# Kernel optimization log

Measured on AMD Instinct MI355X. Metric: run time of the kernel, lower is better.

## Reference

```python
import jax, jax.numpy as jnp
import numpy as np

D_MODEL = 1024
NUM_HEADS = 16
D_K = D_MODEL // NUM_HEADS
ROPE_THETA = 10000.0


def apply_rope(x, pos):
    # x: [B, H, S, d_k], pos: [S] int
    half = x.shape[-1] // 2
    inv_freq = ROPE_THETA ** (-jnp.arange(half, dtype=jnp.float32) * 2.0 / x.shape[-1])
    ang = pos.astype(jnp.float32)[:, None] * inv_freq[None, :]  # [S, half]
    cos, sin = jnp.cos(ang), jnp.sin(ang)
    x1 = x[..., 0::2]
    x2 = x[..., 1::2]
    r1 = x1 * cos - x2 * sin
    r2 = x1 * sin + x2 * cos
    return jnp.stack([r1, r2], axis=-1).reshape(x.shape)


def setup_inputs() -> dict:
    key = jax.random.key(0)
    ks = jax.random.split(key, 5)
    B, S = 4, 2048
    scale = 1.0 / np.sqrt(D_MODEL)
    x = jax.random.normal(ks[0], (B, S, D_MODEL), dtype=jnp.float32)
    w_q = jax.random.normal(ks[1], (D_MODEL, D_MODEL), dtype=jnp.float32) * scale
    w_k = jax.random.normal(ks[2], (D_MODEL, D_MODEL), dtype=jnp.float32) * scale
    w_v = jax.random.normal(ks[3], (D_MODEL, D_MODEL), dtype=jnp.float32) * scale
    w_o = jax.random.normal(ks[4], (D_MODEL, D_MODEL), dtype=jnp.float32) * scale
    token_positions = jnp.arange(S, dtype=jnp.int32)
    return {"x": x, "w_q": w_q, "w_k": w_k, "w_v": w_v, "w_o": w_o, "token_positions": token_positions}


def reference(x, w_q, w_k, w_v, w_o, token_positions):
    B, S, _ = x.shape
    def proj(w):
        return (x @ w.T).reshape(B, S, NUM_HEADS, D_K).transpose(0, 2, 1, 3)  # [B,H,S,d_k]
    q, k, v = proj(w_q), proj(w_k), proj(w_v)
    q = apply_rope(q, token_positions)
    k = apply_rope(k, token_positions)
    logits = jnp.einsum('bhid,bhjd->bhij', q, k) / jnp.sqrt(jnp.float32(D_K))
    causal = jnp.tril(jnp.ones((S, S), dtype=bool))
    logits = jnp.where(causal[None, None], logits, -jnp.inf)
    weights = jax.nn.softmax(logits, axis=-1)
    attn = jnp.einsum('bhij,bhjd->bhid', weights, v)  # [B,H,S,d_k]
    attn = attn.transpose(0, 2, 1, 3).reshape(B, S, D_MODEL)
    return attn @ w_o.T
```

## Files before the change

kernel.cpp:

```cpp
#include <hip/hip_runtime.h>
#include <hip/hip_bf16.h>
#include <stdint.h>

#define DM   1024
#define SEQ  2048
#define BATCH 4
#define NH   16
#define DK   64
#define NTK  16

typedef __attribute__((ext_vector_type(8))) __bf16 bf16x8;
typedef __attribute__((ext_vector_type(4))) float f32x4;
typedef __attribute__((ext_vector_type(4))) unsigned short ushort4_t;
typedef __attribute__((ext_vector_type(4))) unsigned int uint4_t;

typedef __attribute__((address_space(1))) const unsigned int GU32;
typedef __attribute__((address_space(3))) unsigned int LU32;

__device__ inline void gl_lds16(const void* g, void* l) {
  __builtin_amdgcn_global_load_lds((GU32*)g, (LU32*)l, 16, 0, 0);
}

__device__ inline f32x4 mfma16(bf16x8 a, bf16x8 b, f32x4 c) {
  return __builtin_amdgcn_mfma_f32_16x16x32_bf16(a, b, c, 0, 0, 0);
}

__device__ inline unsigned short f2bf(float f) {
  unsigned u = __float_as_uint(f);
  u += 0x7fffu + ((u >> 16) & 1u);
  return (unsigned short)(u >> 16);
}

__device__ inline unsigned cvt_pk_bf16(float a, float b) {
  unsigned r;
  asm("v_cvt_pk_bf16_f32 %0, %1, %2" : "=v"(r) : "v"(a), "v"(b));
  return r;
}

__device__ inline float fexp2(float x) {
  float r;
  asm("v_exp_f32 %0, %1" : "=v"(r) : "v"(x));
  return r;
}

__device__ inline float fmax3(float a, float b, float c) {
  float r;
  asm("v_max3_f32 %0, %1, %2, %3" : "=v"(r) : "v"(a), "v"(b), "v"(c));
  return r;
}

__device__ inline int swz_of(int r) { return ((r & 6) << 2) | ((r & 1) << 5); }
__device__ inline int bswz(int r) { return ((r & 6) << 3) | ((r & 1) << 6); }

__global__ void prep_kernel(const float* __restrict__ x,
                            const float* __restrict__ wq, const float* __restrict__ wk,
                            const float* __restrict__ wv, const float* __restrict__ wo,
                            const int* __restrict__ tp,
                            unsigned short* __restrict__ xbf,
                            unsigned short* __restrict__ wbf,
                            float2* __restrict__ tab)
{
  const int NX4 = (BATCH*SEQ*DM)/4;
  const int NW4 = (DM*DM)/4;
  int idx = blockIdx.x*256 + threadIdx.x;
  if (idx < NX4) {
    float4 v = ((const float4*)x)[idx];
    ushort4_t o; o[0]=f2bf(v.x); o[1]=f2bf(v.y); o[2]=f2bf(v.z); o[3]=f2bf(v.w);
    ((ushort4_t*)xbf)[idx] = o;
  } else if (idx < NX4 + 4*NW4) {
    int t = idx - NX4;
    int wsel = t >> 18;
    int off = t & (NW4-1);
    const float* src = (wsel==0) ? wq : (wsel==1) ? wk : (wsel==2) ? wv : wo;
    float4 v = ((const float4*)src)[off];
    ushort4_t o; o[0]=f2bf(v.x); o[1]=f2bf(v.y); o[2]=f2bf(v.z); o[3]=f2bf(v.w);
    ((ushort4_t*)wbf)[wsel*NW4 + off] = o;
  } else {
    int t = idx - NX4 - 4*NW4;
    if (t < SEQ*32) {
      int s = t >> 5, i = t & 31;
      float invf = exp2f(-(float)i * (13.287712379549449f/32.0f));
      float ang = (float)tp[s] * invf;
      float sn, cs; sincosf(ang, &sn, &cs);
      tab[t] = make_float2(cs, sn);
    }
  }
}

template<int MODE>
__global__ __launch_bounds__(256, 2)
void gemm_db(const unsigned short* __restrict__ A,
             const unsigned short* __restrict__ Wall,
             unsigned short* __restrict__ qbf,
             unsigned short* __restrict__ kbf,
             unsigned short* __restrict__ vt,
             float* __restrict__ ofp,
             const float2* __restrict__ tab)
{
  __shared__ __align__(16) char lds[65536];
  const int tid = threadIdx.x;
  const int bid = blockIdx.x;
  int sel, mt, nt;
  if (MODE == 0) {
    sel = bid >> 9;
    int r = bid & 511;
    int xcd = r & 7, idx = r >> 3;
    mt = xcd*8 + (idx >> 3);  nt = idx & 7;
  } else {
    sel = 3;
    int xcd = bid & 7, idx = bid >> 3;
    mt = xcd*8 + (idx >> 3);  nt = idx & 7;
  }
  const unsigned short* Bm = Wall + (size_t)sel*DM*DM;
  const int a0 = mt*128, b0r = nt*128;
  const int w = tid>>6, lane = tid&63, ln = lane&15, g = lane>>4;
  const int wm = (w>>1)*64, wn = (w&1)*64;

  const char* src[8];
  {
    int rr = tid >> 3;
    int c  = (tid & 7) * 8;
    #pragma unroll
    for (int i = 0; i < 4; ++i) {
      int r_ = i*32 + rr;
      int cs = c ^ swz_of(r_);
      src[i]   = (const char*)(A  + (size_t)(a0  + r_)*DM + cs);
      src[i+4] = (const char*)(Bm + (size_t)(b0r + r_)*DM + cs);
    }
  }

  int offA[4], offB[4];
  #pragma unroll
  for (int m = 0; m < 4; ++m) {
    int R  = wm + m*16 + ln;
    offA[m] = R*128 + ((g*8 ^ swz_of(R)) * 2);
    int Rb = wn + m*16 + ln;
    offB[m] = 16384 + Rb*128 + ((g*8 ^ swz_of(Rb)) * 2);
  }

  f32x4 acc[4][4];
  #pragma unroll
  for (int i=0;i<4;i++)
    #pragma unroll
    for (int j=0;j<4;j++) acc[i][j] = (f32x4){0.f,0.f,0.f,0.f};

  #pragma unroll
  for (int i = 0; i < 8; ++i) gl_lds16(src[i],       lds +         i*4096 + tid*16);
  #pragma unroll
  for (int i = 0; i < 8; ++i) gl_lds16(src[i] + 128, lds + 32768 + i*4096 + tid*16);

  for (int t = 0; t < NTK; ++t) {
    char* sb = lds + (t & 1) * 32768;
    if (t < NTK-1) asm volatile("s_waitcnt vmcnt(8)" ::: "memory");
    else           asm volatile("s_waitcnt vmcnt(0)" ::: "memory");
    __builtin_amdgcn_sched_barrier(0);
    __builtin_amdgcn_s_barrier();
    asm volatile("" ::: "memory");
    __builtin_amdgcn_sched_barrier(0);

    bf16x8 fa[4][2], fb[4][2];
    #pragma unroll
    for (int m = 0; m < 4; ++m) {
      fa[m][0] = *(const bf16x8*)(sb + offA[m]);
      fa[m][1] = *(const bf16x8*)(sb + (offA[m] ^ 64));
      fb[m][0] = *(const bf16x8*)(sb + offB[m]);
      fb[m][1] = *(const bf16x8*)(sb + (offB[m] ^ 64));
    }
    asm volatile("s_waitcnt lgkmcnt(0)" ::: "memory");
    __builtin_amdgcn_sched_barrier(0);
    __builtin_amdgcn_s_barrier();
    asm volatile("" ::: "memory");
    __builtin_amdgcn_sched_barrier(0);

    if (t + 2 < NTK) {
      const int kb = (t + 2) * 128;
      #pragma unroll
      for (int i = 0; i < 8; ++i)
        gl_lds16(src[i] + kb, sb + i*4096 + tid*16);
    }
    __builtin_amdgcn_s_setprio(1);
    #pragma unroll
    for (int h = 0; h < 2; ++h)
      #pragma unroll
      for (int m = 0; m < 4; ++m)
        #pragma unroll
        for (int n = 0; n < 4; ++n)
          acc[m][n] = mfma16(fa[m][h], fb[n][h], acc[m][n]);
    __builtin_amdgcn_s_setprio(0);
  }

  if (MODE == 1) {
    #pragma unroll
    for (int i=0;i<4;i++) {
      int m = a0 + wm + i*16 + g*4;
      #pragma unroll
      for (int jn=0;jn<4;jn++) {
        int n = b0r + wn + jn*16 + ln;
        #pragma unroll
        for (int j=0;j<4;j++)
          ofp[(size_t)(m+j)*DM + n] = acc[i][jn][j];
      }
    }
  } else if (sel == 2) {
    #pragma unroll
    for (int i=0;i<4;i++) {
      int m0 = a0 + wm + i*16 + g*4;
      int bb = m0>>11, s0 = m0&2047;
      #pragma unroll
      for (int jn=0;jn<4;jn++) {
        int n = b0r + wn + jn*16 + ln;
        int h = n>>6, d = n&63;
        ushort4_t o4;
        #pragma unroll
        for (int j=0;j<4;j++) o4[j] = f2bf(acc[i][jn][j]);
        *(ushort4_t*)&vt[(((size_t)bb*NH + h)*DK + d)*SEQ + s0] = o4;
      }
    }
  } else {
    unsigned short* dst = sel ? kbf : qbf;
    const float qs = sel ? 1.0f : 0.1803368802f;
    #pragma unroll
    for (int jn=0;jn<4;jn++) {
      int n = b0r + wn + jn*16 + ln;
      int h = n>>6, d = n&63, di = d>>1, par = d&1;
      #pragma unroll
      for (int i=0;i<4;i++) {
        #pragma unroll
        for (int j=0;j<4;j++) {
          int m = a0 + wm + i*16 + g*4 + j;
          int bb = m>>11, s = m&2047;
          float v = acc[i][jn][j];
          float pv = __shfl_xor(v, 1);
          float2 cssn = tab[s*32 + di];
          float r = par ? (v*cssn.x + pv*cssn.y) : (v*cssn.x - pv*cssn.y);
          dst[((size_t)(bb*NH + h)*SEQ + s)*DK + d] = f2bf(r*qs);
        }
      }
    }
  }
}

__global__ __launch_bounds__(256, 2)
void attn_fa(const unsigned short* __restrict__ qbf,
             const unsigned short* __restrict__ kbf,
             const unsigned short* __restrict__ vtg,
             unsigned short* __restrict__ attnbf)
{
  __shared__ __align__(16) char kv_lds[32768];
  __shared__ unsigned short PlA[4][16][72];
  __shared__ unsigned short PlB[4][16][72];
  const int bh = blockIdx.x, by = blockIdx.y;
  const int qh = 15 - by;
  const int NTa = 2*qh + 2;
  const int NTtot = 34;
  const int tid = threadIdx.x, w = tid>>6, lane = tid&63, ln = lane&15, g = lane>>4;
  const int bb = bh>>4, h = bh&15;

  uint4_t ov = {0x3F803F80u, 0x3F803F80u, 0x3F803F80u, 0x3F803F80u};
  const bf16x8 ones = *(bf16x8*)&ov;

  const int rr = tid >> 3;
  const int cb = (tid & 7) * 16;
  const char* ks0 = (const char*)(kbf + ((size_t)bh*SEQ + rr     )*DK) + (cb ^ bswz(rr));
  const char* ks1 = (const char*)(kbf + ((size_t)bh*SEQ + rr + 32)*DK) + (cb ^ bswz(rr));
  const char* vs0 = (const char*)(vtg + ((size_t)bh*DK  + rr     )*SEQ) + (cb ^ bswz(rr));
  const char* vs1 = (const char*)(vtg + ((size_t)bh*DK  + rr + 32)*SEQ) + (cb ^ bswz(rr));

  const int ok0 = (g*16) ^ bswz(ln);

  gl_lds16(ks0, kv_lds +         tid*16);
  gl_lds16(ks1, kv_lds +  4096 + tid*16);
  gl_lds16(vs0, kv_lds +  8192 + tid*16);
  gl_lds16(vs1, kv_lds + 12288 + tid*16);
  gl_lds16(ks0 + 8192, kv_lds + 16384 +         tid*16);
  gl_lds16(ks1 + 8192, kv_lds + 16384 +  4096 + tid*16);
  gl_lds16(vs0 + 128,  kv_lds + 16384 +  8192 + tid*16);
  gl_lds16(vs1 + 128,  kv_lds + 16384 + 12288 + tid*16);

  int q0a = qh*128 + w*16;
  int q0b = q0a + 64;
  const unsigned short* qrowA = qbf + ((size_t)bh*SEQ + q0a + ln)*DK;
  const unsigned short* qrowB = qbf + ((size_t)bh*SEQ + q0b + ln)*DK;
  bf16x8 qa0 = *(const bf16x8*)(qrowA + g*8);
  bf16x8 qa1 = *(const bf16x8*)(qrowA + 32 + g*8);
  bf16x8 qb0 = *(const bf16x8*)(qrowB + g*8);
  bf16x8 qb1 = *(const bf16x8*)(qrowB + 32 + g*8);

  f32x4 oA[4], oB[4], osA, osB;
  #pragma unroll
  for (int f=0;f<4;f++) { oA[f] = (f32x4){0,0,0,0}; oB[f] = (f32x4){0,0,0,0}; }
  osA = (f32x4){0,0,0,0}; osB = (f32x4){0,0,0,0};
  float mA = -1e30f, mB = -1e30f;

  for (int u = 0; u < NTtot; ++u) {
    const int tloc  = (u < NTa) ? u : u - NTa;
    const int NTcur = (u < NTa) ? NTa : NTtot - NTa;
    char* sb = kv_lds + (u & 1) * 16384;
    if (u < NTtot-1) asm volatile("s_waitcnt vmcnt(4)" ::: "memory");
    else             asm volatile("s_waitcnt vmcnt(0)" ::: "memory");
    __builtin_amdgcn_sched_barrier(0);
    __builtin_amdgcn_s_barrier();
    asm volatile("" ::: "memory");
    __builtin_amdgcn_sched_barrier(0);

    bf16x8 kf[4][2], vfr[4][2];
    #pragma unroll
    for (int a=0;a<4;a++) {
      kf[a][0]  = *(const bf16x8*)(sb + a*2048 + (ok0 ^  0) + ln*128);
      kf[a][1]  = *(const bf16x8*)(sb + a*2048 + (ok0 ^ 64) + ln*128);
      vfr[a][0] = *(const bf16x8*)(sb + 8192 + a*2048 + (ok0 ^  0) + ln*128);
      vfr[a][1] = *(const bf16x8*)(sb + 8192 + a*2048 + (ok0 ^ 64) + ln*128);
    }
    asm volatile("s_waitcnt lgkmcnt(0)" ::: "memory");
    __builtin_amdgcn_sched_barrier(0);
    __builtin_amdgcn_s_barrier();
    asm volatile("" ::: "memory");
    __builtin_amdgcn_sched_barrier(0);

    if (u + 2 < NTtot) {
      const int t2 = (u + 2 < NTa) ? u + 2 : u + 2 - NTa;
      const size_t kO = (size_t)t2*8192, vO = (size_t)t2*128;
      gl_lds16(ks0 + kO, sb +         tid*16);
      gl_lds16(ks1 + kO, sb +  4096 + tid*16);
      gl_lds16(vs0 + vO, sb +  8192 + tid*16);
      gl_lds16(vs1 + vO, sb + 12288 + tid*16);
    }

    if (u == NTa) {
      #pragma unroll
      for (int j=0;j<4;j++) {
        float liA = 1.0f / osA[j];
        float liB = 1.0f / osB[j];
        int sA = q0a + g*4 + j, sB = q0b + g*4 + j;
        #pragma unroll
        for (int f=0;f<4;f++) {
          attnbf[((size_t)bb*SEQ + sA)*DM + h*DK + f*16 + ln] = f2bf(oA[f][j]*liA);
          attnbf[((size_t)bb*SEQ + sB)*DM + h*DK + f*16 + ln] = f2bf(oB[f][j]*liB);
        }
      }
      q0a = by*128 + w*16;
      q0b = q0a + 64;
      const unsigned short* qrA = qbf + ((size_t)bh*SEQ + q0a + ln)*DK;
      const unsigned short* qrB = qbf + ((size_t)bh*SEQ + q0b + ln)*DK;
      qa0 = *(const bf16x8*)(qrA + g*8);
      qa1 = *(const bf16x8*)(qrA + 32 + g*8);
      qb0 = *(const bf16x8*)(qrB + g*8);
      qb1 = *(const bf16x8*)(qrB + 32 + g*8);
      #pragma unroll
      for (int f=0;f<4;f++) { oA[f] = (f32x4){0,0,0,0}; oB[f] = (f32x4){0,0,0,0}; }
      osA = (f32x4){0,0,0,0}; osB = (f32x4){0,0,0,0};
      mA = -1e30f; mB = -1e30f;
    }

    const bool actA = (tloc < NTcur-1);

    f32x4 saA[4], saB[4];
    __builtin_amdgcn_s_setprio(1);
    #pragma unroll
    for (int kvf=0;kvf<4;kvf++) {
      f32x4 zb = (f32x4){0,0,0,0};
      zb = mfma16(kf[kvf][0], qb0, zb);
      zb = mfma16(kf[kvf][1], qb1, zb);
      saB[kvf] = zb;
    }
    if (actA) {
      #pragma unroll
      for (int kvf=0;kvf<4;kvf++) {
        f32x4 za = (f32x4){0,0,0,0};
        za = mfma16(kf[kvf][0], qa0, za);
        za = mfma16(kf[kvf][1], qa1, za);
        saA[kvf] = za;
      }
    }
    __builtin_amdgcn_s_setprio(0);

    if (actA) {
      if (tloc == NTcur-2) {
        int thr = q0a + ln - tloc*64 - g*4;
        #pragma unroll
        for (int kvf=0;kvf<4;kvf++)
          #pragma unroll
          for (int j=0;j<4;j++)
            if (kvf*16 + j > thr) saA[kvf][j] = -1e30f;
      }
      float lm = fmax3(saA[0][0], saA[0][1], saA[0][2]);
      lm = fmax3(lm, saA[0][3], saA[1][0]);
      lm = fmax3(lm, saA[1][1], saA[1][2]);
      lm = fmax3(lm, saA[1][3], saA[2][0]);
      lm = fmax3(lm, saA[2][1], saA[2][2]);
      lm = fmax3(lm, saA[2][3], saA[3][0]);
      lm = fmax3(lm, saA[3][1], saA[3][2]);
      lm = fmaxf(lm, saA[3][3]);
      lm = fmaxf(lm, __shfl_xor(lm, 16));
      lm = fmaxf(lm, __shfl_xor(lm, 32));
      if (!__all(lm - mA <= 8.0f)) {
        float mnew = fmaxf(mA, lm);
        float corr = fexp2(mA - mnew);
        #pragma unroll
        for (int j=0;j<4;j++) {
          float cj = __shfl(corr, g*4 + j);
          #pragma unroll
          for (int f=0;f<4;f++) oA[f][j] *= cj;
          osA[j] *= cj;
        }
        mA = mnew;
      }
      #pragma unroll
      for (int kvf=0;kvf<4;kvf++) {
        float p0 = fexp2(saA[kvf][0] - mA);
        float p1 = fexp2(saA[kvf][1] - mA);
        float p2 = fexp2(saA[kvf][2] - mA);
        float p3 = fexp2(saA[kvf][3] - mA);
        uint2 pk;
        pk.x = cvt_pk_bf16(p0, p1);
        pk.y = cvt_pk_bf16(p2, p3);
        *(uint2*)&PlA[w][ln][kvf*16 + g*4] = pk;
      }
    }

    {
      if (tloc == NTcur-1) {
        int thr = q0b + ln - tloc*64 - g*4;
        #pragma unroll
        for (int kvf=0;kvf<4;kvf++)
          #pragma unroll
          for (int j=0;j<4;j++)
            if (kvf*16 + j > thr) saB[kvf][j] = -1e30f;
      }
      float lm = fmax3(saB[0][0], saB[0][1], saB[0][2]);
      lm = fmax3(lm, saB[0][3], saB[1][0]);
      lm = fmax3(lm, saB[1][1], saB[1][2]);
      lm = fmax3(lm, saB[1][3], saB[2][0]);
      lm = fmax3(lm, saB[2][1], saB[2][2]);
      lm = fmax3(lm, saB[2][3], saB[3][0]);
      lm = fmax3(lm, saB[3][1], saB[3][2]);
      lm = fmaxf(lm, saB[3][3]);
      lm = fmaxf(lm, __shfl_xor(lm, 16));
      lm = fmaxf(lm, __shfl_xor(lm, 32));
      if (!__all(lm - mB <= 8.0f)) {
        float mnew = fmaxf(mB, lm);
        float corr = fexp2(mB - mnew);
        #pragma unroll
        for (int j=0;j<4;j++) {
          float cj = __shfl(corr, g*4 + j);
          #pragma unroll
          for (int f=0;f<4;f++) oB[f][j] *= cj;
          osB[j] *= cj;
        }
        mB = mnew;
      }
      #pragma unroll
      for (int kvf=0;kvf<4;kvf++) {
        float p0 = fexp2(saB[kvf][0] - mB);
        float p1 = fexp2(saB[kvf][1] - mB);
        float p2 = fexp2(saB[kvf][2] - mB);
        float p3 = fexp2(saB[kvf][3] - mB);
        uint2 pk;
        pk.x = cvt_pk_bf16(p0, p1);
        pk.y = cvt_pk_bf16(p2, p3);
        *(uint2*)&PlB[w][ln][kvf*16 + g*4] = pk;
      }
    }

    asm volatile("s_waitcnt lgkmcnt(0)" ::: "memory");

    __builtin_amdgcn_s_setprio(1);
    #pragma unroll
    for (int c=0;c<2;c++) {
      bf16x8 pfB = *(const bf16x8*)&PlB[w][ln][c*32 + g*8];
      #pragma unroll
      for (int f=0;f<4;f++)
        oB[f] = mfma16(pfB, vfr[f][c], oB[f]);
      osB = mfma16(pfB, ones, osB);
    }
    if (actA) {
      #pragma unroll
      for (int c=0;c<2;c++) {
        bf16x8 pfA = *(const bf16x8*)&PlA[w][ln][c*32 + g*8];
        #pragma unroll
        for (int f=0;f<4;f++)
          oA[f] = mfma16(pfA, vfr[f][c], oA[f]);
        osA = mfma16(pfA, ones, osA);
      }
    }
    __builtin_amdgcn_s_setprio(0);
  }

  #pragma unroll
  for (int j=0;j<4;j++) {
    float liA = 1.0f / osA[j];
    float liB = 1.0f / osB[j];
    int sA = q0a + g*4 + j, sB = q0b + g*4 + j;
    #pragma unroll
    for (int f=0;f<4;f++) {
      attnbf[((size_t)bb*SEQ + sA)*DM + h*DK + f*16 + ln] = f2bf(oA[f][j]*liA);
      attnbf[((size_t)bb*SEQ + sB)*DM + h*DK + f*16 + ln] = f2bf(oB[f][j]*liB);
    }
  }
}

extern "C" void kernel_launch(void* const* d_in, const int* in_sizes, int n_in,
                              void* d_out, int out_size, void* d_ws, size_t ws_size,
                              hipStream_t stream)
{
  const float* x  = (const float*)d_in[0];
  const float* wq = (const float*)d_in[1];
  const float* wk = (const float*)d_in[2];
  const float* wv = (const float*)d_in[3];
  const float* wo = (const float*)d_in[4];
  const int*   tp = (const int*)d_in[5];

  const size_t XB = (size_t)BATCH*SEQ*DM*2;
  const size_t WB = (size_t)DM*DM*2;

  char* ws = (char*)d_ws;
  unsigned short* xbf = (unsigned short*)(ws);
  unsigned short* qbf = (unsigned short*)(ws + XB);
  unsigned short* kbf = (unsigned short*)(ws + 2*XB);
  unsigned short* vt  = (unsigned short*)(ws + 3*XB);
  unsigned short* abf = (unsigned short*)(ws + 4*XB);
  unsigned short* wbf = (unsigned short*)(ws + 5*XB);
  float2* tab = (float2*)(ws + 5*XB + 4*WB);

  prep_kernel<<<12544, 256, 0, stream>>>(x, wq, wk, wv, wo, tp, xbf, wbf, tab);

  gemm_db<0><<<1536, 256, 0, stream>>>(xbf, wbf, qbf, kbf, vt, nullptr, tab);
  attn_fa<<<dim3(64,8), 256, 0, stream>>>(qbf, kbf, vt, abf);
  gemm_db<1><<<512, 256, 0, stream>>>(abf, wbf, nullptr, nullptr, nullptr,
                                      (float*)d_out, nullptr);
}
```

Before: 174.8 us.

## Restructure causal attention into 64-row query blocks with 2-wave workgroups

The attention kernel moves from 256-thread blocks covering paired 128-row query blocks to 128-thread blocks covering paired 64-row query blocks, launched on a 64x16 grid. Each wave now holds two adjacent 16-row query tiles, so the per-tile active/inactive branch goes away and only the diagonal tile is masked. The P staging buffer becomes one swizzled LDS region per wave that the A and B tiles reuse one after the other, with their PV products interleaved. The aim is finer load balancing, less wasted causal work and smaller LDS use, at the cost of more K/V loads per thread and more serialisation between the two softmax halves.

```diff
diff --git a/kernel.cpp b/kernel.cpp
--- a/kernel.cpp
+++ b/kernel.cpp
@@ -240,19 +240,18 @@
   }
 }
 
-__global__ __launch_bounds__(256, 2)
+__global__ __launch_bounds__(128, 2)
 void attn_fa(const unsigned short* __restrict__ qbf,
              const unsigned short* __restrict__ kbf,
              const unsigned short* __restrict__ vtg,
              unsigned short* __restrict__ attnbf)
 {
   __shared__ __align__(16) char kv_lds[32768];
-  __shared__ unsigned short PlA[4][16][72];
-  __shared__ unsigned short PlB[4][16][72];
-  const int bh = blockIdx.x, by = blockIdx.y;
-  const int qh = 15 - by;
-  const int NTa = 2*qh + 2;
-  const int NTtot = 34;
+  __shared__ __align__(16) char pl_lds[4096];
+  const int bh = blockIdx.x, pr = blockIdx.y;
+  const int qbA = 31 - pr;
+  const int NTa = qbA + 1;
+  const int NTtot = 33;
   const int tid = threadIdx.x, w = tid>>6, lane = tid&63, ln = lane&15, g = lane>>4;
   const int bb = bh>>4, h = bh&15;
 
@@ -261,30 +260,37 @@
 
   const int rr = tid >> 3;
   const int cb = (tid & 7) * 16;
-  const char* ks0 = (const char*)(kbf + ((size_t)bh*SEQ + rr     )*DK) + (cb ^ bswz(rr));
-  const char* ks1 = (const char*)(kbf + ((size_t)bh*SEQ + rr + 32)*DK) + (cb ^ bswz(rr));
-  const char* vs0 = (const char*)(vtg + ((size_t)bh*DK  + rr     )*SEQ) + (cb ^ bswz(rr));
-  const char* vs1 = (const char*)(vtg + ((size_t)bh*DK  + rr + 32)*SEQ) + (cb ^ bswz(rr));
+  const char* ks[4]; const char* vs[4];
+  #pragma unroll
+  for (int i = 0; i < 4; ++i) {
+    int row = rr + i*16;
+    ks[i] = (const char*)(kbf + ((size_t)bh*SEQ + row)*DK) + (cb ^ bswz(row));
+    vs[i] = (const char*)(vtg + ((size_t)bh*DK  + row)*SEQ) + (cb ^ bswz(row));
+  }
 
   const int ok0 = (g*16) ^ bswz(ln);
-
-  gl_lds16(ks0, kv_lds +         tid*16);
-  gl_lds16(ks1, kv_lds +  4096 + tid*16);
-  gl_lds16(vs0, kv_lds +  8192 + tid*16);
-  gl_lds16(vs1, kv_lds + 12288 + tid*16);
-  gl_lds16(ks0 + 8192, kv_lds + 16384 +         tid*16);
-  gl_lds16(ks1 + 8192, kv_lds + 16384 +  4096 + tid*16);
-  gl_lds16(vs0 + 128,  kv_lds + 16384 +  8192 + tid*16);
-  gl_lds16(vs1 + 128,  kv_lds + 16384 + 12288 + tid*16);
-
-  int q0a = qh*128 + w*16;
-  int q0b = q0a + 64;
-  const unsigned short* qrowA = qbf + ((size_t)bh*SEQ + q0a + ln)*DK;
-  const unsigned short* qrowB = qbf + ((size_t)bh*SEQ + q0b + ln)*DK;
-  bf16x8 qa0 = *(const bf16x8*)(qrowA + g*8);
-  bf16x8 qa1 = *(const bf16x8*)(qrowA + 32 + g*8);
-  bf16x8 qb0 = *(const bf16x8*)(qrowB + g*8);
-  bf16x8 qb1 = *(const bf16x8*)(qrowB + 32 + g*8);
+  char* plw = pl_lds + w*2048 + ln*128;
+  const int plswz = (ln & 7) << 4;
+
+  #pragma unroll
+  for (int i = 0; i < 4; ++i) {
+    gl_lds16(ks[i], kv_lds + i*2048 + tid*16);
+    gl_lds16(vs[i], kv_lds + 8192 + i*2048 + tid*16);
+  }
+  #pragma unroll
+  for (int i = 0; i < 4; ++i) {
+    gl_lds16(ks[i] + 8192, kv_lds + 16384 + i*2048 + tid*16);
+    gl_lds16(vs[i] + 128,  kv_lds + 16384 + 8192 + i*2048 + tid*16);
+  }
+
+  int q0a = qbA*64 + w*32;
+  int q0b = q0a + 16;
+  const unsigned short* qrA = qbf + ((size_t)bh*SEQ + q0a + ln)*DK;
+  const unsigned short* qrB = qbf + ((size_t)bh*SEQ + q0b + ln)*DK;
+  bf16x8 qa0 = *(const bf16x8*)(qrA + g*8);
+  bf16x8 qa1 = *(const bf16x8*)(qrA + 32 + g*8);
+  bf16x8 qb0 = *(const bf16x8*)(qrB + g*8);
+  bf16x8 qb1 = *(const bf16x8*)(qrB + 32 + g*8);
 
   f32x4 oA[4], oB[4], osA, osB;
   #pragma unroll
@@ -296,7 +302,7 @@
     const int tloc  = (u < NTa) ? u : u - NTa;
     const int NTcur = (u < NTa) ? NTa : NTtot - NTa;
     char* sb = kv_lds + (u & 1) * 16384;
-    if (u < NTtot-1) asm volatile("s_waitcnt vmcnt(4)" ::: "memory");
+    if (u < NTtot-1) asm volatile("s_waitcnt vmcnt(8)" ::: "memory");
     else             asm volatile("s_waitcnt vmcnt(0)" ::: "memory");
     __builtin_amdgcn_sched_barrier(0);
     __builtin_amdgcn_s_barrier();
@@ -320,10 +326,11 @@
     if (u + 2 < NTtot) {
       const int t2 = (u + 2 < NTa) ? u + 2 : u + 2 - NTa;
       const size_t kO = (size_t)t2*8192, vO = (size_t)t2*128;
-      gl_lds16(ks0 + kO, sb +         tid*16);
-      gl_lds16(ks1 + kO, sb +  4096 + tid*16);
-      gl_lds16(vs0 + vO, sb +  8192 + tid*16);
-      gl_lds16(vs1 + vO, sb + 12288 + tid*16);
+      #pragma unroll
+      for (int i = 0; i < 4; ++i) {
+        gl_lds16(ks[i] + kO, sb + i*2048 + tid*16);
+        gl_lds16(vs[i] + vO, sb + 8192 + i*2048 + tid*16);
+      }
     }
 
     if (u == NTa) {
@@ -338,44 +345,39 @@
           attnbf[((size_t)bb*SEQ + sB)*DM + h*DK + f*16 + ln] = f2bf(oB[f][j]*liB);
         }
       }
-      q0a = by*128 + w*16;
-      q0b = q0a + 64;
-      const unsigned short* qrA = qbf + ((size_t)bh*SEQ + q0a + ln)*DK;
-      const unsigned short* qrB = qbf + ((size_t)bh*SEQ + q0b + ln)*DK;
-      qa0 = *(const bf16x8*)(qrA + g*8);
-      qa1 = *(const bf16x8*)(qrA + 32 + g*8);
-      qb0 = *(const bf16x8*)(qrB + g*8);
-      qb1 = *(const bf16x8*)(qrB + 32 + g*8);
+      q0a = pr*64 + w*32;
+      q0b = q0a + 16;
+      const unsigned short* qa = qbf + ((size_t)bh*SEQ + q0a + ln)*DK;
+      const unsigned short* qb = qbf + ((size_t)bh*SEQ + q0b + ln)*DK;
+      qa0 = *(const bf16x8*)(qa + g*8);
+      qa1 = *(const bf16x8*)(qa + 32 + g*8);
+      qb0 = *(const bf16x8*)(qb + g*8);
+      qb1 = *(const bf16x8*)(qb + 32 + g*8);
       #pragma unroll
       for (int f=0;f<4;f++) { oA[f] = (f32x4){0,0,0,0}; oB[f] = (f32x4){0,0,0,0}; }
       osA = (f32x4){0,0,0,0}; osB = (f32x4){0,0,0,0};
       mA = -1e30f; mB = -1e30f;
     }
 
-    const bool actA = (tloc < NTcur-1);
-
     f32x4 saA[4], saB[4];
     __builtin_amdgcn_s_setprio(1);
     #pragma unroll
     for (int kvf=0;kvf<4;kvf++) {
+      f32x4 za = (f32x4){0,0,0,0};
+      za = mfma16(kf[kvf][0], qa0, za);
+      za = mfma16(kf[kvf][1], qa1, za);
+      saA[kvf] = za;
       f32x4 zb = (f32x4){0,0,0,0};
       zb = mfma16(kf[kvf][0], qb0, zb);
       zb = mfma16(kf[kvf][1], qb1, zb);
       saB[kvf] = zb;
     }
-    if (actA) {
-      #pragma unroll
-      for (int kvf=0;kvf<4;kvf++) {
-        f32x4 za = (f32x4){0,0,0,0};
-        za = mfma16(kf[kvf][0], qa0, za);
-        za = mfma16(kf[kvf][1], qa1, za);
-        saA[kvf] = za;
-      }
-    }
     __builtin_amdgcn_s_setprio(0);
 
-    if (actA) {
-      if (tloc == NTcur-2) {
+    const bool diag = (tloc == NTcur-1);
+
+    {
+      if (diag) {
         int thr = q0a + ln - tloc*64 - g*4;
         #pragma unroll
         for (int kvf=0;kvf<4;kvf++)
@@ -414,12 +416,22 @@
         uint2 pk;
         pk.x = cvt_pk_bf16(p0, p1);
         pk.y = cvt_pk_bf16(p2, p3);
-        *(uint2*)&PlA[w][ln][kvf*16 + g*4] = pk;
+        *(uint2*)(plw + ((kvf*32 + g*8) ^ plswz)) = pk;
+      }
+      asm volatile("s_waitcnt lgkmcnt(0)" ::: "memory");
+      __builtin_amdgcn_sched_barrier(0);
+      #pragma unroll
+      for (int c=0;c<2;c++) {
+        bf16x8 pfA = *(const bf16x8*)(plw + ((c*64 + g*16) ^ plswz));
+        #pragma unroll
+        for (int f=0;f<4;f++)
+          oA[f] = mfma16(pfA, vfr[f][c], oA[f]);
+        osA = mfma16(pfA, ones, osA);
       }
     }
 
     {
-      if (tloc == NTcur-1) {
+      if (diag) {
         int thr = q0b + ln - tloc*64 - g*4;
         #pragma unroll
         for (int kvf=0;kvf<4;kvf++)
@@ -458,32 +470,21 @@
         uint2 pk;
         pk.x = cvt_pk_bf16(p0, p1);
         pk.y = cvt_pk_bf16(p2, p3);
-        *(uint2*)&PlB[w][ln][kvf*16 + g*4] = pk;
-      }
-    }
-
-    asm volatile("s_waitcnt lgkmcnt(0)" ::: "memory");
-
-    __builtin_amdgcn_s_setprio(1);
-    #pragma unroll
-    for (int c=0;c<2;c++) {
-      bf16x8 pfB = *(const bf16x8*)&PlB[w][ln][c*32 + g*8];
-      #pragma unroll
-      for (int f=0;f<4;f++)
-        oB[f] = mfma16(pfB, vfr[f][c], oB[f]);
-      osB = mfma16(pfB, ones, osB);
-    }
-    if (actA) {
+        *(uint2*)(plw + ((kvf*32 + g*8) ^ plswz)) = pk;
+      }
+      asm volatile("s_waitcnt lgkmcnt(0)" ::: "memory");
+      __builtin_amdgcn_sched_barrier(0);
+      __builtin_amdgcn_s_setprio(1);
       #pragma unroll
       for (int c=0;c<2;c++) {
-        bf16x8 pfA = *(const bf16x8*)&PlA[w][ln][c*32 + g*8];
+        bf16x8 pfB = *(const bf16x8*)(plw + ((c*64 + g*16) ^ plswz));
         #pragma unroll
         for (int f=0;f<4;f++)
-          oA[f] = mfma16(pfA, vfr[f][c], oA[f]);
-        osA = mfma16(pfA, ones, osA);
-      }
-    }
-    __builtin_amdgcn_s_setprio(0);
+          oB[f] = mfma16(pfB, vfr[f][c], oB[f]);
+        osB = mfma16(pfB, ones, osB);
+      }
+      __builtin_amdgcn_s_setprio(0);
+    }
   }
 
   #pragma unroll
@@ -525,7 +526,7 @@
   prep_kernel<<<12544, 256, 0, stream>>>(x, wq, wk, wv, wo, tp, xbf, wbf, tab);
 
   gemm_db<0><<<1536, 256, 0, stream>>>(xbf, wbf, qbf, kbf, vt, nullptr, tab);
-  attn_fa<<<dim3(64,8), 256, 0, stream>>>(qbf, kbf, vt, abf);
+  attn_fa<<<dim3(64,16), 128, 0, stream>>>(qbf, kbf, vt, abf);
   gemm_db<1><<<512, 256, 0, stream>>>(abf, wbf, nullptr, nullptr, nullptr,
                                       (float*)d_out, nullptr);
 }
```

Measured after the change: 175.4 us. No clear change (+0.4%).
